# Kernel tuning notes

Hardware: AMD Instinct MI355X
Metric: run time of the kernel (lower is better)

## Reference

```python
import jax, jax.numpy as jnp
import numpy as np

N = 256          # num agents
HID = 128        # hidden_dim
ACT = 5          # action_dim
NH = 4           # num_heads
D = HID + 16     # concat_hidden_dim = 144
E = D * NH       # mha embed dim = 576
HD = D           # per-head dim = E // NH = 144
OBS_RX, OBS_RY = 4, 2   # obs_r from fov_size=(9,5)
GRID = 40


def setup_inputs() -> dict:
    key = jax.random.key(0)
    ks = jax.random.split(key, 24)
    g = lambda k, shape, s: (jax.random.normal(k, shape, dtype=jnp.float32) * s)
    inp = {
        "hidden_state_n": g(ks[0], (N, HID), 1.0),
        "action_n": g(ks[1], (N, HID), 1.0),
        "state_n": jax.random.randint(ks[2], (N, 2), 0, GRID, dtype=jnp.int32),
        # obs encoder
        "W_enc": g(ks[3], (HID, 16), HID ** -0.5), "b_enc": jnp.zeros((16,), jnp.float32),
        # MHABlock outer projections
        "Wq": g(ks[4], (D, E), D ** -0.5), "bq": jnp.zeros((E,), jnp.float32),
        "Wk": g(ks[5], (D, E), D ** -0.5), "bk": jnp.zeros((E,), jnp.float32),
        "Wv": g(ks[6], (D, E), D ** -0.5), "bv": jnp.zeros((E,), jnp.float32),
        # nn.MultiheadAttention internal in/out projections
        "Wiq": g(ks[7], (E, E), E ** -0.5), "biq": jnp.zeros((E,), jnp.float32),
        "Wik": g(ks[8], (E, E), E ** -0.5), "bik": jnp.zeros((E,), jnp.float32),
        "Wiv": g(ks[9], (E, E), E ** -0.5), "biv": jnp.zeros((E,), jnp.float32),
        "Wo_proj": g(ks[10], (E, E), E ** -0.5), "bo_proj": jnp.zeros((E,), jnp.float32),
        "W_O": g(ks[11], (E, D), E ** -0.5),  # no bias
        # dueling decoders
        "W_val": g(ks[12], (D, 1), D ** -0.5), "b_val": jnp.zeros((1,), jnp.float32),
        "W_adv": g(ks[13], (D, ACT), D ** -0.5), "b_adv": jnp.zeros((ACT,), jnp.float32),
    }
    return inp


def reference(hidden_state_n, action_n, W_enc, b_enc, Wq, bq, Wk, bk, Wv, bv,
              Wiq, biq, Wik, bik, Wiv, biv, Wo_proj, bo_proj, W_O,
              W_val, b_val, W_adv, b_adv, state_n):
    n = hidden_state_n.shape[0]
    # observed_agents[i] = {j > i : |x_i-x_j|<=rx and |y_i-y_j|<=ry}
    pos = state_n.astype(jnp.int32)
    dx = jnp.abs(pos[:, None, 0] - pos[None, :, 0])
    dy = jnp.abs(pos[:, None, 1] - pos[None, :, 1])
    upper = jnp.arange(n)[None, :] > jnp.arange(n)[:, None]
    mask = (dx <= OBS_RX) & (dy <= OBS_RY) & upper            # [N,N], mask[i,j]: j observed by i

    # per-neighbor feature c_j = concat(obs_encoder(h_j), a_j)  -> [N, D]
    obs = hidden_state_n @ W_enc + b_enc                       # [N,16]
    C = jnp.concatenate([obs, action_n], axis=-1)              # [N,D]

    # MHABlock: outer Q/K/V projections then nn.MultiheadAttention
    q = (C @ Wq + bq) @ Wiq + biq                              # [N,E]
    k = (C @ Wk + bk) @ Wik + bik
    v = (C @ Wv + bv) @ Wiv + biv
    q2 = q.reshape(n, NH, HD)
    k2 = k.reshape(n, NH, HD)
    v2 = v.reshape(n, NH, HD)

    scale = 1.0 / np.sqrt(HD).astype(np.float32)
    S = jnp.einsum("jhd,khd->hjk", q2, k2) * scale             # [H,N,N] shared across agents

    pair = (mask[:, None, :, None] & mask[:, None, None, :])   # [N,1,Nq,Nk]
    logits = jnp.where(pair, S[None, :, :, :], -1e9)           # [N,H,N,N]
    m = jnp.max(logits, axis=-1, keepdims=True)
    p = jnp.exp(logits - m) * pair.astype(logits.dtype)
    attn = p / jnp.maximum(p.sum(axis=-1, keepdims=True), 1e-9)

    ctx = jnp.einsum("ihjk,khd->ijhd", attn, v2).reshape(n, n, E)  # [N,Nq,E]
    out = (ctx @ Wo_proj + bo_proj) @ W_O                          # [N,Nq,D]

    # sum over the (masked) neighbor/query axis -> per-agent h_i
    h = jnp.sum(out * mask[:, :, None].astype(out.dtype), axis=1)  # [N,D]

    V = h @ W_val + b_val                                          # [N,1]
    A = h @ W_adv + b_adv                                          # [N,ACT]
    Q = V + A - jnp.mean(A, axis=-1, keepdims=True)                # dueling Q
    return Q
```

## Files before the change

### kernel.cpp

```cpp
#include <hip/hip_runtime.h>
#include <hip/hip_bf16.h>

typedef __hip_bfloat16 bf16;

#define NAG 256
#define HID 128
#define ACT 5
#define NH 4
#define DD 144
#define EE 576
#define HDIM 144
#define CMAX 20

template<int KDIM, int AG, int NX, int GSLOTS>
__global__ __launch_bounds__(256) void k_gemmK(
    const float* __restrict__ A0, const float* __restrict__ A1, const float* __restrict__ A2,
    const bf16* __restrict__ W0, const bf16* __restrict__ W1, const bf16* __restrict__ W2,
    const float* __restrict__ bb0, const float* __restrict__ bb1, const float* __restrict__ bb2,
    const float* __restrict__ bscale,
    float* __restrict__ o0, float* __restrict__ o1, float* __restrict__ o2,
    int N)
{
    constexpr int Kc = KDIM / 4;
    constexpr int G  = 36;
    constexpr int NG = Kc / G;
    constexpr int LDA = KDIM + 4;
    __shared__ union { float As[8 * LDA]; float red[2048]; } sm;

    const int p = blockIdx.x;
    const int xcd = p & 7, qq = p >> 3;
    const int mb = qq & 31, gslot = qq >> 5;
    const int g = xcd + 8 * gslot;
    if (g >= AG) return;
    const int bx = g % NX, z = g / NX;
    const float* A   = (z == 0) ? A0  : (z == 1) ? A1  : A2;
    const bf16*  W   = (z == 0) ? W0  : (z == 1) ? W1  : W2;
    const float* bia = (z == 0) ? bb0 : (z == 1) ? bb1 : bb2;
    float*       out = (z == 0) ? o0  : (z == 1) ? o1  : o2;
    const int tid = threadIdx.x;

    for (int idx = tid; idx < 8 * (KDIM / 4); idx += 256) {
        int r = idx / (KDIM / 4), c = idx % (KDIM / 4);
        *((float4*)&sm.As[r * LDA + c * 4]) =
            *(const float4*)(A + (size_t)(mb * 8 + r) * KDIM + c * 4);
    }
    __syncthreads();

    const int wave = tid >> 6, lane = tid & 63;
    const int colg = bx * 64 + lane;
    const bool cv = colg < N;
    const int colc = cv ? colg : (N - 1);
    const bf16* Wp = W + (size_t)(wave * Kc) * N + colc;
    float acc[8] = {};
    float wv[G], wn[G];
    #pragma unroll
    for (int j = 0; j < G; ++j) wv[j] = __bfloat162float(Wp[(size_t)j * N]);
    for (int gi = 0; gi < NG; ++gi) {
        if (gi + 1 < NG) {
            const bf16* Wn = Wp + (size_t)(gi + 1) * G * N;
            #pragma unroll
            for (int j = 0; j < G; ++j) wn[j] = __bfloat162float(Wn[(size_t)j * N]);
        }
        const int kb = wave * Kc + gi * G;
        #pragma unroll
        for (int j4 = 0; j4 < G / 4; ++j4) {
            #pragma unroll
            for (int r = 0; r < 8; ++r) {
                float4 a4 = *(const float4*)&sm.As[r * LDA + kb + j4 * 4];
                acc[r] += a4.x * wv[j4 * 4 + 0] + a4.y * wv[j4 * 4 + 1]
                        + a4.z * wv[j4 * 4 + 2] + a4.w * wv[j4 * 4 + 3];
            }
        }
        #pragma unroll
        for (int j = 0; j < G; ++j) wv[j] = wn[j];
    }
    __syncthreads();
    #pragma unroll
    for (int r = 0; r < 8; ++r) sm.red[wave * 512 + r * 64 + lane] = acc[r];
    __syncthreads();
    #pragma unroll
    for (int q = 0; q < 2; ++q) {
        int idx = tid + q * 256;
        int r = idx >> 6, cl = idx & 63;
        int col = bx * 64 + cl;
        if (col < N) {
            float s = sm.red[idx] + sm.red[512 + idx]
                    + sm.red[1024 + idx] + sm.red[1536 + idx];
            int row = mb * 8 + r;
            float bs = bscale ? bscale[row] : 1.f;
            float bb = bia ? bia[col] : 0.f;
            out[(size_t)row * N + col] = s + bs * bb;
        }
    }
}

__global__ __launch_bounds__(256) void k_gemm1(
    const float* __restrict__ hidden, const float* __restrict__ action,
    const float* __restrict__ W_enc, const float* __restrict__ b_enc,
    const float* __restrict__ Wq, const float* __restrict__ Wk, const float* __restrict__ Wv,
    const float* __restrict__ bq, const float* __restrict__ bk, const float* __restrict__ bv,
    const float* __restrict__ Wiq, const float* __restrict__ Wik, const float* __restrict__ Wiv,
    const float* __restrict__ Wo, const float* __restrict__ W_O,
    float* __restrict__ tq, float* __restrict__ tk, float* __restrict__ tv,
    bf16* __restrict__ Wbiq, bf16* __restrict__ Wbik, bf16* __restrict__ Wbiv,
    bf16* __restrict__ Wbo, bf16* __restrict__ WbO)
{
    const int p = blockIdx.x;
    const int xcd = p & 7, qq = p >> 3;
    const int mb = qq & 31, gslot = qq >> 5;
    const int g = xcd + 8 * gslot;
    const int tid = threadIdx.x;
    if (g >= 27) {
        const int wb = (g - 27) * 32 + mb;
        const int CH = 8832;
        for (int i = wb * CH + tid; i < (wb + 1) * CH; i += 256) {
            if (i >= 1410048) break;
            if (i < 331776)        Wbiq[i]           = __float2bfloat16(Wiq[i]);
            else if (i < 663552)   Wbik[i - 331776]  = __float2bfloat16(Wik[i - 331776]);
            else if (i < 995328)   Wbiv[i - 663552]  = __float2bfloat16(Wiv[i - 663552]);
            else if (i < 1327104)  Wbo[i - 995328]   = __float2bfloat16(Wo[i - 995328]);
            else                   WbO[i - 1327104]  = __float2bfloat16(W_O[i - 1327104]);
        }
        return;
    }
    const int bx = g % 9, z = g / 9;
    const float* W  = (z == 0) ? Wq : (z == 1) ? Wk : Wv;
    const float* bi = (z == 0) ? bq : (z == 1) ? bk : bv;
    float*      out = (z == 0) ? tq : (z == 1) ? tk : tv;

    __shared__ float Ct[8][148];
    __shared__ union { struct { float Hs[8][132]; float We[2048]; } e;
                       float red[2048]; } u;
    {
        int r = tid >> 5, kq = tid & 31;
        *((float4*)&u.e.Hs[r][kq * 4]) =
            *(const float4*)(hidden + (mb * 8 + r) * HID + kq * 4);
        *((float4*)&Ct[r][16 + kq * 4]) =
            *(const float4*)(action + (mb * 8 + r) * HID + kq * 4);
        *((float4*)&u.e.We[tid * 4])        = *(const float4*)(W_enc + tid * 4);
        *((float4*)&u.e.We[1024 + tid * 4]) = *(const float4*)(W_enc + 1024 + tid * 4);
    }
    __syncthreads();
    if (tid < 128) {
        int r = tid >> 4, o = tid & 15;
        float acc = 0.f;
        #pragma unroll 8
        for (int d = 0; d < HID; ++d) acc += u.e.Hs[r][d] * u.e.We[d * 16 + o];
        Ct[r][o] = acc + b_enc[o];
    }
    __syncthreads();

    constexpr int Kc = 36, G = 36;
    const int wave = tid >> 6, lane = tid & 63;
    const int colg = bx * 64 + lane;
    const float* Wp = W + (size_t)(wave * Kc) * EE + colg;
    float acc[8] = {};
    float wv[G];
    #pragma unroll
    for (int j = 0; j < G; ++j) wv[j] = Wp[(size_t)j * EE];
    const int kb = wave * Kc;
    #pragma unroll
    for (int j4 = 0; j4 < G / 4; ++j4) {
        #pragma unroll
        for (int r = 0; r < 8; ++r) {
            float4 a4 = *(const float4*)&Ct[r][kb + j4 * 4];
            acc[r] += a4.x * wv[j4 * 4 + 0] + a4.y * wv[j4 * 4 + 1]
                    + a4.z * wv[j4 * 4 + 2] + a4.w * wv[j4 * 4 + 3];
        }
    }
    __syncthreads();
    #pragma unroll
    for (int r = 0; r < 8; ++r) u.red[wave * 512 + r * 64 + lane] = acc[r];
    __syncthreads();
    #pragma unroll
    for (int q = 0; q < 2; ++q) {
        int idx = tid + q * 256;
        int r = idx >> 6, cl = idx & 63;
        int col = bx * 64 + cl;
        float s = u.red[idx] + u.red[512 + idx]
                + u.red[1024 + idx] + u.red[1536 + idx];
        out[(size_t)(mb * 8 + r) * EE + col] = s + bi[col];
    }
}

__global__ __launch_bounds__(256) void k_attn(
    const int* __restrict__ state, const float* __restrict__ q,
    const float* __restrict__ kmat, const float* __restrict__ v,
    float* __restrict__ ctxsum, float* __restrict__ cnt)
{
    __shared__ int lst[NAG];
    __shared__ int cnt_s;
    __shared__ float w4[NH][NAG];
    __shared__ float qh[CMAX][HDIM + 1];
    __shared__ float kh[CMAX][HDIM + 1];
    __shared__ float Sl[CMAX][CMAX + 1];
    const int i = blockIdx.x, tid = threadIdx.x;
    if (tid == 0) cnt_s = 0;
    __syncthreads();
    {
        int xi = state[2 * i], yi = state[2 * i + 1];
        int xj = state[2 * tid], yj = state[2 * tid + 1];
        int dx = xi - xj; if (dx < 0) dx = -dx;
        int dy = yi - yj; if (dy < 0) dy = -dy;
        if (tid > i && dx <= 4 && dy <= 2) {
            int p = atomicAdd(&cnt_s, 1);
            lst[p] = tid;
        }
    }
    __syncthreads();
    const int c = cnt_s;
    if (tid == 0) cnt[i] = (float)c;
    if (c == 0) {
        for (int e = tid; e < EE; e += 256) ctxsum[i * EE + e] = 0.f;
        return;
    }
    if (c <= CMAX) {
        for (int h = 0; h < NH; ++h) {
            for (int idx = tid; idx < c * HDIM; idx += 256) {
                int jj = idx / HDIM, d = idx % HDIM;
                qh[jj][d] = q[lst[jj] * EE + h * HDIM + d];
                kh[jj][d] = kmat[lst[jj] * EE + h * HDIM + d];
            }
            __syncthreads();
            for (int pp = tid; pp < c * c; pp += 256) {
                int jj = pp / c, kk = pp % c;
                float acc = 0.f;
                for (int d = 0; d < HDIM; ++d) acc += qh[jj][d] * kh[kk][d];
                Sl[jj][kk] = acc * (1.0f / 12.0f);
            }
            __syncthreads();
            if (tid < c) {
                float m = -1e30f;
                for (int kk = 0; kk < c; ++kk) m = fmaxf(m, Sl[tid][kk]);
                float zz = 0.f;
                for (int kk = 0; kk < c; ++kk) zz += __expf(Sl[tid][kk] - m);
                float inv = 1.f / fmaxf(zz, 1e-9f);
                for (int kk = 0; kk < c; ++kk)
                    Sl[tid][kk] = __expf(Sl[tid][kk] - m) * inv;
            }
            __syncthreads();
            if (tid < c) {
                float s = 0.f;
                for (int jj = 0; jj < c; ++jj) s += Sl[jj][tid];
                w4[h][tid] = s;
            }
            __syncthreads();
        }
    } else {
        for (int idx = tid; idx < NH * c; idx += 256) w4[idx / c][idx % c] = 0.f;
        __syncthreads();
        for (int pnh = tid; pnh < NH * c; pnh += 256) {
            int h = pnh / c, jj = pnh % c;
            const float* qrow = q + lst[jj] * EE + h * HDIM;
            float m = -1e30f;
            for (int kk = 0; kk < c; ++kk) {
                const float* krow = kmat + lst[kk] * EE + h * HDIM;
                float a = 0.f;
                for (int d = 0; d < HDIM; ++d) a += qrow[d] * krow[d];
                m = fmaxf(m, a * (1.0f / 12.0f));
            }
            float zz = 0.f;
            for (int kk = 0; kk < c; ++kk) {
                const float* krow = kmat + lst[kk] * EE + h * HDIM;
                float a = 0.f;
                for (int d = 0; d < HDIM; ++d) a += qrow[d] * krow[d];
                zz += __expf(a * (1.0f / 12.0f) - m);
            }
            float inv = 1.f / fmaxf(zz, 1e-9f);
            for (int kk = 0; kk < c; ++kk) {
                const float* krow = kmat + lst[kk] * EE + h * HDIM;
                float a = 0.f;
                for (int d = 0; d < HDIM; ++d) a += qrow[d] * krow[d];
                atomicAdd(&w4[h][kk], __expf(a * (1.0f / 12.0f) - m) * inv);
            }
        }
        __syncthreads();
    }
    for (int e = tid; e < EE; e += 256) {
        int h = e / HDIM;
        float a0 = 0.f, a1 = 0.f;
        int t = 0;
        for (; t + 1 < c; t += 2) {
            a0 += w4[h][t] * v[lst[t] * EE + e];
            a1 += w4[h][t + 1] * v[lst[t + 1] * EE + e];
        }
        if (t < c) a0 += w4[h][t] * v[lst[t] * EE + e];
        ctxsum[i * EE + e] = a0 + a1;
    }
}

__global__ __launch_bounds__(256) void k_tail(
    const float* __restrict__ tout, const bf16* __restrict__ WbO,
    const float* __restrict__ W_val, const float* __restrict__ b_val,
    const float* __restrict__ W_adv, const float* __restrict__ b_adv,
    float* __restrict__ out)
{
    __shared__ float As[4][EE];
    __shared__ float hb[4][DD];
    const int b = blockIdx.x, tid = threadIdx.x;
    const int a0 = b * 4;
    for (int idx = tid; idx < 4 * (EE / 4); idx += 256) {
        int r = idx / (EE / 4), c4 = idx % (EE / 4);
        *((float4*)&As[r][c4 * 4]) =
            *(const float4*)(tout + (size_t)(a0 + r) * EE + c4 * 4);
    }
    __syncthreads();
    if (tid < DD) {
        const int col = tid;
        const bf16* Wp = WbO + col;
        float ac0 = 0.f, ac1 = 0.f, ac2 = 0.f, ac3 = 0.f;
        float wv[32], wn[32];
        #pragma unroll
        for (int j = 0; j < 32; ++j) wv[j] = __bfloat162float(Wp[(size_t)j * DD]);
        for (int gI = 0; gI < 18; ++gI) {
            if (gI + 1 < 18) {
                const bf16* Wn = Wp + (size_t)(gI + 1) * 32 * DD;
                #pragma unroll
                for (int j = 0; j < 32; ++j) wn[j] = __bfloat162float(Wn[(size_t)j * DD]);
            }
            const int kb = gI * 32;
            #pragma unroll
            for (int j = 0; j < 32; ++j) {
                float w = wv[j];
                ac0 += As[0][kb + j] * w; ac1 += As[1][kb + j] * w;
                ac2 += As[2][kb + j] * w; ac3 += As[3][kb + j] * w;
            }
            #pragma unroll
            for (int j = 0; j < 32; ++j) wv[j] = wn[j];
        }
        hb[0][col] = ac0; hb[1][col] = ac1; hb[2][col] = ac2; hb[3][col] = ac3;
    }
    __syncthreads();
    const int wave = tid >> 6, lane = tid & 63;
    float h0 = hb[wave][lane], h1 = hb[wave][lane + 64];
    float h2 = (lane < 16) ? hb[wave][lane + 128] : 0.f;
    float red[6];
    for (int o = 0; o < 6; ++o) {
        float p;
        if (o < 5) {
            p = h0 * W_adv[lane * ACT + o] + h1 * W_adv[(lane + 64) * ACT + o];
            if (lane < 16) p += h2 * W_adv[(lane + 128) * ACT + o];
        } else {
            p = h0 * W_val[lane] + h1 * W_val[lane + 64];
            if (lane < 16) p += h2 * W_val[lane + 128];
        }
        for (int off = 32; off; off >>= 1) p += __shfl_xor(p, off);
        red[o] = p;
    }
    if (lane == 0) {
        float a[ACT], mean = 0.f;
        for (int o = 0; o < ACT; ++o) { a[o] = red[o] + b_adv[o]; mean += a[o]; }
        mean *= (1.0f / ACT);
        float V = red[5] + b_val[0];
        for (int o = 0; o < ACT; ++o) out[(a0 + wave) * ACT + o] = V + a[o] - mean;
    }
}

extern "C" void kernel_launch(void* const* d_in, const int* in_sizes, int n_in,
                              void* d_out, int out_size, void* d_ws, size_t ws_size,
                              hipStream_t stream)
{
    const float* hidden = (const float*)d_in[0];
    const float* action = (const float*)d_in[1];
    const int*   state  = (const int*)d_in[2];

    float* ws = (float*)d_ws;
    float* tq   = ws;
    float* tk   = tq   + NAG * EE;
    float* tv   = tk   + NAG * EE;
    float* q    = tv   + NAG * EE;
    float* kb   = q    + NAG * EE;
    float* v    = kb   + NAG * EE;
    float* ctx  = v    + NAG * EE;
    float* cnt  = ctx  + NAG * EE;
    bf16*  bw   = (bf16*)(cnt + NAG);
    bf16*  Wbiq = bw;
    bf16*  Wbik = Wbiq + 331776;
    bf16*  Wbiv = Wbik + 331776;
    bf16*  Wbo  = Wbiv + 331776;
    bf16*  WbO  = Wbo  + 331776;
    float* tout = tq;

    k_gemm1<<<1024, 256, 0, stream>>>(hidden, action,
        (const float*)d_in[3], (const float*)d_in[4],
        (const float*)d_in[5], (const float*)d_in[7], (const float*)d_in[9],
        (const float*)d_in[6], (const float*)d_in[8], (const float*)d_in[10],
        (const float*)d_in[11], (const float*)d_in[13], (const float*)d_in[15],
        (const float*)d_in[17], (const float*)d_in[19],
        tq, tk, tv, Wbiq, Wbik, Wbiv, Wbo, WbO);

    k_gemmK<576, 27, 9, 4><<<1024, 256, 0, stream>>>(tq, tk, tv,
        Wbiq, Wbik, Wbiv,
        (const float*)d_in[12], (const float*)d_in[14], (const float*)d_in[16],
        nullptr, q, kb, v, EE);

    k_attn<<<NAG, 256, 0, stream>>>(state, q, kb, v, ctx, cnt);

    k_gemmK<576, 9, 9, 2><<<512, 256, 0, stream>>>(ctx, ctx, ctx,
        Wbo, Wbo, Wbo,
        (const float*)d_in[18], (const float*)d_in[18], (const float*)d_in[18],
        cnt, tout, tout, tout, EE);

    k_tail<<<64, 256, 0, stream>>>(tout, WbO,
        (const float*)d_in[20], (const float*)d_in[21],
        (const float*)d_in[22], (const float*)d_in[23], (float*)d_out);
}
```

Baseline: 212.6 us.

## Pre-multiply chained weight matrices to collapse back-to-back linear projections

Exploits associativity to fold the outer projections into the attention in-projections (Wq·Wiq etc.) and Wo_proj·W_O into single combined weights with folded biases, computed each call in a prep kernel. The per-agent 576x576 GEMMs become 144x576 GEMMs, and the separate output-projection GEMM is removed because the tail applies the combined 576x144 weight directly, with a count-scaled bias. The bf16 weight conversion is dropped in favour of fp32 weights, which doubles weight bytes but removes a conversion pass and a full GEMM stage. The weight products cost roughly as much as one of the removed GEMMs per call.

Result: faster. 191.9 us (-9.8%).

```diff
diff --git a/kernel.cpp b/kernel.cpp
--- a/kernel.cpp
+++ b/kernel.cpp
@@ -1,7 +1,5 @@
 #include <hip/hip_runtime.h>
 #include <hip/hip_bf16.h>
-
-typedef __hip_bfloat16 bf16;
 
 #define NAG 256
 #define HID 128
@@ -12,158 +10,187 @@
 #define HDIM 144
 #define CMAX 20
 
-template<int KDIM, int AG, int NX, int GSLOTS>
-__global__ __launch_bounds__(256) void k_gemmK(
-    const float* __restrict__ A0, const float* __restrict__ A1, const float* __restrict__ A2,
-    const bf16* __restrict__ W0, const bf16* __restrict__ W1, const bf16* __restrict__ W2,
-    const float* __restrict__ bb0, const float* __restrict__ bb1, const float* __restrict__ bb2,
-    const float* __restrict__ bscale,
-    float* __restrict__ o0, float* __restrict__ o1, float* __restrict__ o2,
-    int N)
-{
-    constexpr int Kc = KDIM / 4;
-    constexpr int G  = 36;
-    constexpr int NG = Kc / G;
-    constexpr int LDA = KDIM + 4;
-    __shared__ union { float As[8 * LDA]; float red[2048]; } sm;
-
-    const int p = blockIdx.x;
-    const int xcd = p & 7, qq = p >> 3;
-    const int mb = qq & 31, gslot = qq >> 5;
-    const int g = xcd + 8 * gslot;
-    if (g >= AG) return;
-    const int bx = g % NX, z = g / NX;
-    const float* A   = (z == 0) ? A0  : (z == 1) ? A1  : A2;
-    const bf16*  W   = (z == 0) ? W0  : (z == 1) ? W1  : W2;
-    const float* bia = (z == 0) ? bb0 : (z == 1) ? bb1 : bb2;
-    float*       out = (z == 0) ? o0  : (z == 1) ? o1  : o2;
-    const int tid = threadIdx.x;
-
-    for (int idx = tid; idx < 8 * (KDIM / 4); idx += 256) {
-        int r = idx / (KDIM / 4), c = idx % (KDIM / 4);
-        *((float4*)&sm.As[r * LDA + c * 4]) =
-            *(const float4*)(A + (size_t)(mb * 8 + r) * KDIM + c * 4);
-    }
-    __syncthreads();
-
+__device__ __forceinline__ void prod_tile(
+    const float* __restrict__ A, const float* __restrict__ W,
+    float* __restrict__ out, int rowbase, int colbase, int N,
+    int tid, float* sm)
+{
+    const int LDA = 580;
+    float* As = sm;
+    for (int idx = tid; idx < 8 * 144; idx += 256) {
+        int r = idx / 144, c = idx % 144;
+        *((float4*)&As[r * LDA + c * 4]) =
+            *(const float4*)(A + (size_t)(rowbase + r) * 576 + c * 4);
+    }
+    __syncthreads();
     const int wave = tid >> 6, lane = tid & 63;
-    const int colg = bx * 64 + lane;
-    const bool cv = colg < N;
-    const int colc = cv ? colg : (N - 1);
-    const bf16* Wp = W + (size_t)(wave * Kc) * N + colc;
+    const int colg = colbase + lane;
+    const int colc = (colg < N) ? colg : (N - 1);
+    const float* Wp = W + (size_t)(wave * 144) * N + colc;
     float acc[8] = {};
-    float wv[G], wn[G];
-    #pragma unroll
-    for (int j = 0; j < G; ++j) wv[j] = __bfloat162float(Wp[(size_t)j * N]);
-    for (int gi = 0; gi < NG; ++gi) {
-        if (gi + 1 < NG) {
-            const bf16* Wn = Wp + (size_t)(gi + 1) * G * N;
+    float wv[36], wn[36];
+    #pragma unroll
+    for (int j = 0; j < 36; ++j) wv[j] = Wp[(size_t)j * N];
+    for (int gi = 0; gi < 4; ++gi) {
+        if (gi + 1 < 4) {
+            const float* Wn = Wp + (size_t)(gi + 1) * 36 * N;
             #pragma unroll
-            for (int j = 0; j < G; ++j) wn[j] = __bfloat162float(Wn[(size_t)j * N]);
-        }
-        const int kb = wave * Kc + gi * G;
+            for (int j = 0; j < 36; ++j) wn[j] = Wn[(size_t)j * N];
+        }
+        const int kb = wave * 144 + gi * 36;
         #pragma unroll
-        for (int j4 = 0; j4 < G / 4; ++j4) {
+        for (int j4 = 0; j4 < 9; ++j4) {
             #pragma unroll
             for (int r = 0; r < 8; ++r) {
-                float4 a4 = *(const float4*)&sm.As[r * LDA + kb + j4 * 4];
+                float4 a4 = *(const float4*)&As[r * LDA + kb + j4 * 4];
                 acc[r] += a4.x * wv[j4 * 4 + 0] + a4.y * wv[j4 * 4 + 1]
                         + a4.z * wv[j4 * 4 + 2] + a4.w * wv[j4 * 4 + 3];
             }
         }
         #pragma unroll
-        for (int j = 0; j < G; ++j) wv[j] = wn[j];
-    }
-    __syncthreads();
-    #pragma unroll
-    for (int r = 0; r < 8; ++r) sm.red[wave * 512 + r * 64 + lane] = acc[r];
+        for (int j = 0; j < 36; ++j) wv[j] = wn[j];
+    }
+    __syncthreads();
+    float* red = sm;
+    #pragma unroll
+    for (int r = 0; r < 8; ++r) red[wave * 512 + r * 64 + lane] = acc[r];
     __syncthreads();
     #pragma unroll
     for (int q = 0; q < 2; ++q) {
         int idx = tid + q * 256;
         int r = idx >> 6, cl = idx & 63;
-        int col = bx * 64 + cl;
+        int col = colbase + cl;
         if (col < N) {
-            float s = sm.red[idx] + sm.red[512 + idx]
-                    + sm.red[1024 + idx] + sm.red[1536 + idx];
-            int row = mb * 8 + r;
-            float bs = bscale ? bscale[row] : 1.f;
-            float bb = bia ? bia[col] : 0.f;
-            out[(size_t)row * N + col] = s + bs * bb;
-        }
-    }
-}
-
-__global__ __launch_bounds__(256) void k_gemm1(
+            float s = red[idx] + red[512 + idx] + red[1024 + idx] + red[1536 + idx];
+            out[(size_t)(rowbase + r) * N + col] = s;
+        }
+    }
+}
+
+__global__ __launch_bounds__(256) void k_pre(
     const float* __restrict__ hidden, const float* __restrict__ action,
     const float* __restrict__ W_enc, const float* __restrict__ b_enc,
     const float* __restrict__ Wq, const float* __restrict__ Wk, const float* __restrict__ Wv,
     const float* __restrict__ bq, const float* __restrict__ bk, const float* __restrict__ bv,
     const float* __restrict__ Wiq, const float* __restrict__ Wik, const float* __restrict__ Wiv,
-    const float* __restrict__ Wo, const float* __restrict__ W_O,
-    float* __restrict__ tq, float* __restrict__ tk, float* __restrict__ tv,
-    bf16* __restrict__ Wbiq, bf16* __restrict__ Wbik, bf16* __restrict__ Wbiv,
-    bf16* __restrict__ Wbo, bf16* __restrict__ WbO)
+    const float* __restrict__ biq, const float* __restrict__ bik, const float* __restrict__ biv,
+    const float* __restrict__ Wo, const float* __restrict__ bo, const float* __restrict__ W_O,
+    float* __restrict__ C,
+    float* __restrict__ Wqc, float* __restrict__ Wkc, float* __restrict__ Wvc,
+    float* __restrict__ Wc,
+    float* __restrict__ bqc, float* __restrict__ bkc, float* __restrict__ bvc,
+    float* __restrict__ bvec)
+{
+    __shared__ float sm[4640];
+    const int p = blockIdx.x, tid = threadIdx.x;
+    if (p < 576) {
+        const int xcd = p & 7, r = p >> 3;
+        const int gslot = r / 18, mb = r % 18;
+        const int g = xcd + 8 * gslot;
+        if (g >= 27) return;
+        const int bx = g % 9, z = g / 9;
+        const float* A = (z == 0) ? Wq  : (z == 1) ? Wk  : Wv;
+        const float* W = (z == 0) ? Wiq : (z == 1) ? Wik : Wiv;
+        float*     out = (z == 0) ? Wqc : (z == 1) ? Wkc : Wvc;
+        prod_tile(A, W, out, mb * 8, bx * 64, EE, tid, sm);
+    } else if (p < 1152) {
+        const int pp = p - 576;
+        const int xcd = pp & 7, mb = pp >> 3;
+        if (xcd >= 3) return;
+        prod_tile(Wo, W_O, Wc, mb * 8, xcd * 64, DD, tid, sm);
+    } else if (p < 1184) {
+        const int mb = p - 1152;
+        float* Hs = sm;
+        float* We = sm + 1056;
+        {
+            int r = tid >> 5, kq = tid & 31;
+            *((float4*)&Hs[r * 132 + kq * 4]) =
+                *(const float4*)(hidden + (mb * 8 + r) * HID + kq * 4);
+            float4 a4 = *(const float4*)(action + (mb * 8 + r) * HID + kq * 4);
+            *((float4*)(C + (size_t)(mb * 8 + r) * DD + 16 + kq * 4)) = a4;
+            *((float4*)&We[tid * 4])        = *(const float4*)(W_enc + tid * 4);
+            *((float4*)&We[1024 + tid * 4]) = *(const float4*)(W_enc + 1024 + tid * 4);
+        }
+        __syncthreads();
+        if (tid < 128) {
+            int r = tid >> 4, o = tid & 15;
+            float acc = 0.f;
+            #pragma unroll 8
+            for (int d = 0; d < HID; ++d) acc += Hs[r * 132 + d] * We[d * 16 + o];
+            C[(size_t)(mb * 8 + r) * DD + o] = acc + b_enc[o];
+        }
+    } else {
+        const int t = p - 1184;
+        const float *bsel, *W, *badd;
+        float* out;
+        int N, bx;
+        if (t < 27) {
+            int z = t / 9; bx = t % 9; N = EE;
+            bsel = (z == 0) ? bq  : (z == 1) ? bk  : bv;
+            W    = (z == 0) ? Wiq : (z == 1) ? Wik : Wiv;
+            badd = (z == 0) ? biq : (z == 1) ? bik : biv;
+            out  = (z == 0) ? bqc : (z == 1) ? bkc : bvc;
+        } else {
+            bx = t - 27; N = DD;
+            bsel = bo; W = W_O; badd = nullptr; out = bvec;
+        }
+        float* bs = sm;
+        float* red = sm + 576;
+        for (int i = tid; i < 144; i += 256)
+            *((float4*)&bs[i * 4]) = *(const float4*)(bsel + i * 4);
+        __syncthreads();
+        const int wave = tid >> 6, lane = tid & 63;
+        const int colg = bx * 64 + lane;
+        const int colc = (colg < N) ? colg : (N - 1);
+        float acc = 0.f;
+        for (int k = wave * 144; k < wave * 144 + 144; ++k)
+            acc += bs[k] * W[(size_t)k * N + colc];
+        red[wave * 64 + lane] = acc;
+        __syncthreads();
+        if (tid < 64 && bx * 64 + tid < N) {
+            float s = red[tid] + red[64 + tid] + red[128 + tid] + red[192 + tid];
+            out[bx * 64 + tid] = s + (badd ? badd[bx * 64 + tid] : 0.f);
+        }
+    }
+}
+
+__global__ __launch_bounds__(256) void k_qkv(
+    const float* __restrict__ C,
+    const float* __restrict__ Wqc, const float* __restrict__ Wkc, const float* __restrict__ Wvc,
+    const float* __restrict__ bqc, const float* __restrict__ bkc, const float* __restrict__ bvc,
+    float* __restrict__ q, float* __restrict__ kb, float* __restrict__ v)
 {
     const int p = blockIdx.x;
     const int xcd = p & 7, qq = p >> 3;
     const int mb = qq & 31, gslot = qq >> 5;
     const int g = xcd + 8 * gslot;
+    if (g >= 27) return;
+    const int bx = g % 9, z = g / 9;
+    const float* W  = (z == 0) ? Wqc : (z == 1) ? Wkc : Wvc;
+    const float* bi = (z == 0) ? bqc : (z == 1) ? bkc : bvc;
+    float*      out = (z == 0) ? q   : (z == 1) ? kb  : v;
     const int tid = threadIdx.x;
-    if (g >= 27) {
-        const int wb = (g - 27) * 32 + mb;
-        const int CH = 8832;
-        for (int i = wb * CH + tid; i < (wb + 1) * CH; i += 256) {
-            if (i >= 1410048) break;
-            if (i < 331776)        Wbiq[i]           = __float2bfloat16(Wiq[i]);
-            else if (i < 663552)   Wbik[i - 331776]  = __float2bfloat16(Wik[i - 331776]);
-            else if (i < 995328)   Wbiv[i - 663552]  = __float2bfloat16(Wiv[i - 663552]);
-            else if (i < 1327104)  Wbo[i - 995328]   = __float2bfloat16(Wo[i - 995328]);
-            else                   WbO[i - 1327104]  = __float2bfloat16(W_O[i - 1327104]);
-        }
-        return;
-    }
-    const int bx = g % 9, z = g / 9;
-    const float* W  = (z == 0) ? Wq : (z == 1) ? Wk : Wv;
-    const float* bi = (z == 0) ? bq : (z == 1) ? bk : bv;
-    float*      out = (z == 0) ? tq : (z == 1) ? tk : tv;
-
-    __shared__ float Ct[8][148];
-    __shared__ union { struct { float Hs[8][132]; float We[2048]; } e;
-                       float red[2048]; } u;
-    {
-        int r = tid >> 5, kq = tid & 31;
-        *((float4*)&u.e.Hs[r][kq * 4]) =
-            *(const float4*)(hidden + (mb * 8 + r) * HID + kq * 4);
-        *((float4*)&Ct[r][16 + kq * 4]) =
-            *(const float4*)(action + (mb * 8 + r) * HID + kq * 4);
-        *((float4*)&u.e.We[tid * 4])        = *(const float4*)(W_enc + tid * 4);
-        *((float4*)&u.e.We[1024 + tid * 4]) = *(const float4*)(W_enc + 1024 + tid * 4);
-    }
-    __syncthreads();
-    if (tid < 128) {
-        int r = tid >> 4, o = tid & 15;
-        float acc = 0.f;
-        #pragma unroll 8
-        for (int d = 0; d < HID; ++d) acc += u.e.Hs[r][d] * u.e.We[d * 16 + o];
-        Ct[r][o] = acc + b_enc[o];
-    }
-    __syncthreads();
-
-    constexpr int Kc = 36, G = 36;
+
+    __shared__ union { float As[8 * 148]; float red[2048]; } u;
+    for (int idx = tid; idx < 8 * 36; idx += 256) {
+        int r = idx / 36, c = idx % 36;
+        *((float4*)&u.As[r * 148 + c * 4]) =
+            *(const float4*)(C + (size_t)(mb * 8 + r) * DD + c * 4);
+    }
+    __syncthreads();
     const int wave = tid >> 6, lane = tid & 63;
     const int colg = bx * 64 + lane;
-    const float* Wp = W + (size_t)(wave * Kc) * EE + colg;
+    const float* Wp = W + (size_t)(wave * 36) * EE + colg;
     float acc[8] = {};
-    float wv[G];
-    #pragma unroll
-    for (int j = 0; j < G; ++j) wv[j] = Wp[(size_t)j * EE];
-    const int kb = wave * Kc;
-    #pragma unroll
-    for (int j4 = 0; j4 < G / 4; ++j4) {
+    float wv[36];
+    #pragma unroll
+    for (int j = 0; j < 36; ++j) wv[j] = Wp[(size_t)j * EE];
+    const int kbase = wave * 36;
+    #pragma unroll
+    for (int j4 = 0; j4 < 9; ++j4) {
         #pragma unroll
         for (int r = 0; r < 8; ++r) {
-            float4 a4 = *(const float4*)&Ct[r][kb + j4 * 4];
+            float4 a4 = *(const float4*)&u.As[r * 148 + kbase + j4 * 4];
             acc[r] += a4.x * wv[j4 * 4 + 0] + a4.y * wv[j4 * 4 + 1]
                     + a4.z * wv[j4 * 4 + 2] + a4.w * wv[j4 * 4 + 3];
         }
@@ -173,8 +200,8 @@
     for (int r = 0; r < 8; ++r) u.red[wave * 512 + r * 64 + lane] = acc[r];
     __syncthreads();
     #pragma unroll
-    for (int q = 0; q < 2; ++q) {
-        int idx = tid + q * 256;
+    for (int qi = 0; qi < 2; ++qi) {
+        int idx = tid + qi * 256;
         int r = idx >> 6, cl = idx & 63;
         int col = bx * 64 + cl;
         float s = u.red[idx] + u.red[512 + idx]
@@ -290,7 +317,8 @@
 }
 
 __global__ __launch_bounds__(256) void k_tail(
-    const float* __restrict__ tout, const bf16* __restrict__ WbO,
+    const float* __restrict__ ctx, const float* __restrict__ Wc,
+    const float* __restrict__ cnt, const float* __restrict__ bvec,
     const float* __restrict__ W_val, const float* __restrict__ b_val,
     const float* __restrict__ W_adv, const float* __restrict__ b_adv,
     float* __restrict__ out)
@@ -302,33 +330,37 @@
     for (int idx = tid; idx < 4 * (EE / 4); idx += 256) {
         int r = idx / (EE / 4), c4 = idx % (EE / 4);
         *((float4*)&As[r][c4 * 4]) =
-            *(const float4*)(tout + (size_t)(a0 + r) * EE + c4 * 4);
+            *(const float4*)(ctx + (size_t)(a0 + r) * EE + c4 * 4);
     }
     __syncthreads();
     if (tid < DD) {
         const int col = tid;
-        const bf16* Wp = WbO + col;
+        const float* Wp = Wc + col;
         float ac0 = 0.f, ac1 = 0.f, ac2 = 0.f, ac3 = 0.f;
         float wv[32], wn[32];
         #pragma unroll
-        for (int j = 0; j < 32; ++j) wv[j] = __bfloat162float(Wp[(size_t)j * DD]);
+        for (int j = 0; j < 32; ++j) wv[j] = Wp[(size_t)j * DD];
         for (int gI = 0; gI < 18; ++gI) {
             if (gI + 1 < 18) {
-                const bf16* Wn = Wp + (size_t)(gI + 1) * 32 * DD;
+                const float* Wn = Wp + (size_t)(gI + 1) * 32 * DD;
                 #pragma unroll
-                for (int j = 0; j < 32; ++j) wn[j] = __bfloat162float(Wn[(size_t)j * DD]);
-            }
-            const int kb = gI * 32;
+                for (int j = 0; j < 32; ++j) wn[j] = Wn[(size_t)j * DD];
+            }
+            const int kbase = gI * 32;
             #pragma unroll
             for (int j = 0; j < 32; ++j) {
                 float w = wv[j];
-                ac0 += As[0][kb + j] * w; ac1 += As[1][kb + j] * w;
-                ac2 += As[2][kb + j] * w; ac3 += As[3][kb + j] * w;
+                ac0 += As[0][kbase + j] * w; ac1 += As[1][kbase + j] * w;
+                ac2 += As[2][kbase + j] * w; ac3 += As[3][kbase + j] * w;
             }
             #pragma unroll
             for (int j = 0; j < 32; ++j) wv[j] = wn[j];
         }
-        hb[0][col] = ac0; hb[1][col] = ac1; hb[2][col] = ac2; hb[3][col] = ac3;
+        float bvc = bvec[col];
+        hb[0][col] = ac0 + cnt[a0 + 0] * bvc;
+        hb[1][col] = ac1 + cnt[a0 + 1] * bvc;
+        hb[2][col] = ac2 + cnt[a0 + 2] * bvc;
+        hb[3][col] = ac3 + cnt[a0 + 3] * bvc;
     }
     __syncthreads();
     const int wave = tid >> 6, lane = tid & 63;
@@ -365,43 +397,35 @@
     const int*   state  = (const int*)d_in[2];
 
     float* ws = (float*)d_ws;
-    float* tq   = ws;
-    float* tk   = tq   + NAG * EE;
-    float* tv   = tk   + NAG * EE;
-    float* q    = tv   + NAG * EE;
+    float* C    = ws;
+    float* Wqc  = C    + NAG * DD;
+    float* Wkc  = Wqc  + DD * EE;
+    float* Wvc  = Wkc  + DD * EE;
+    float* Wc   = Wvc  + DD * EE;
+    float* bqc  = Wc   + EE * DD;
+    float* bkc  = bqc  + EE;
+    float* bvc  = bkc  + EE;
+    float* bvec = bvc  + EE;
+    float* q    = bvec + DD;
     float* kb   = q    + NAG * EE;
     float* v    = kb   + NAG * EE;
     float* ctx  = v    + NAG * EE;
     float* cnt  = ctx  + NAG * EE;
-    bf16*  bw   = (bf16*)(cnt + NAG);
-    bf16*  Wbiq = bw;
-    bf16*  Wbik = Wbiq + 331776;
-    bf16*  Wbiv = Wbik + 331776;
-    bf16*  Wbo  = Wbiv + 331776;
-    bf16*  WbO  = Wbo  + 331776;
-    float* tout = tq;
-
-    k_gemm1<<<1024, 256, 0, stream>>>(hidden, action,
+
+    k_pre<<<1214, 256, 0, stream>>>(hidden, action,
         (const float*)d_in[3], (const float*)d_in[4],
         (const float*)d_in[5], (const float*)d_in[7], (const float*)d_in[9],
         (const float*)d_in[6], (const float*)d_in[8], (const float*)d_in[10],
         (const float*)d_in[11], (const float*)d_in[13], (const float*)d_in[15],
-        (const float*)d_in[17], (const float*)d_in[19],
-        tq, tk, tv, Wbiq, Wbik, Wbiv, Wbo, WbO);
-
-    k_gemmK<576, 27, 9, 4><<<1024, 256, 0, stream>>>(tq, tk, tv,
-        Wbiq, Wbik, Wbiv,
         (const float*)d_in[12], (const float*)d_in[14], (const float*)d_in[16],
-        nullptr, q, kb, v, EE);
+        (const float*)d_in[17], (const float*)d_in[18], (const float*)d_in[19],
+        C, Wqc, Wkc, Wvc, Wc, bqc, bkc, bvc, bvec);
+
+    k_qkv<<<1024, 256, 0, stream>>>(C, Wqc, Wkc, Wvc, bqc, bkc, bvc, q, kb, v);
 
     k_attn<<<NAG, 256, 0, stream>>>(state, q, kb, v, ctx, cnt);
 
-    k_gemmK<576, 9, 9, 2><<<512, 256, 0, stream>>>(ctx, ctx, ctx,
-        Wbo, Wbo, Wbo,
-        (const float*)d_in[18], (const float*)d_in[18], (const float*)d_in[18],
-        cnt, tout, tout, tout, EE);
-
-    k_tail<<<64, 256, 0, stream>>>(tout, WbO,
+    k_tail<<<64, 256, 0, stream>>>(ctx, Wc, cnt, bvec,
         (const float*)d_in[20], (const float*)d_in[21],
         (const float*)d_in[22], (const float*)d_in[23], (float*)d_out);
 }
```
